# Performance work log

Measured on AMD Instinct MI355X. Metric: run time of the kernel, lower is better.

The kernel has to match this reference:

```python
import jax, jax.numpy as jnp
import numpy as np

BS, L, H, D = 4, 1024, 12, 768   # docs, seq len, attn heads, hidden
NE, M, P = 42, 96, 42 * 42        # max entities (min_height), mentions/doc, ht pairs
OFFSET = 1                        # bert/roberta [CLS] offset


def setup_inputs() -> dict:
    key = jax.random.key(0)
    k1, k2, k3, k4, k5 = jax.random.split(key, 5)
    sequence_output = jax.random.normal(k1, (BS, L, D), jnp.float32)
    attention = jax.random.uniform(k2, (BS, H, L, L), jnp.float32)
    mention_pos = jax.random.randint(k3, (BS, M), 0, L - OFFSET - 1).astype(jnp.int32)
    mention_entity = jnp.sort(jax.random.randint(k4, (BS, M), 0, NE), axis=-1).astype(jnp.int32)
    hts = jax.random.randint(k5, (BS, P, 2), 0, NE).astype(jnp.int32)
    return {"sequence_output": sequence_output, "attention": attention,
            "mention_pos": mention_pos, "mention_entity": mention_entity, "hts": hts}


def _per_doc_entities(seq, att, pos, ent):
    # seq [L,D], att [H,L,L], pos [M] mention token idx, ent [M] entity segment id
    idx = pos + OFFSET
    m_emb = seq[idx]                              # [M,D]  gathered mention embeddings
    m_att = jnp.transpose(att[:, idx], (1, 0, 2))  # [M,H,L] gathered mention attentions
    counts = jax.ops.segment_sum(jnp.ones((M,), seq.dtype), ent, num_segments=NE)
    has = counts > 0
    # mean-pool attentions per entity (zeros for empty entities, as in torch code)
    e_att = jax.ops.segment_sum(m_att, ent, num_segments=NE) / jnp.maximum(counts, 1.0)[:, None, None]
    # stable logsumexp-pool embeddings per entity
    seg_max = jax.ops.segment_max(m_emb, ent, num_segments=NE)      # -inf for empty segments
    seg_max = jnp.where(has[:, None], seg_max, 0.0)
    seg_sum = jax.ops.segment_sum(jnp.exp(m_emb - seg_max[ent]), ent, num_segments=NE)
    e_emb = jnp.where(has[:, None], jnp.log(jnp.maximum(seg_sum, 1e-30)) + seg_max, 0.0)
    return e_emb, e_att                           # [NE,D], [NE,H,L]


def _channel_map(seq, e_att):
    # all-pairs (h_att * t_att).mean(heads), normalize over tokens, contract with seq
    pair = jnp.einsum('ahl,bhl->abl', e_att, e_att) / H      # [NE,NE,L]
    pair = pair / (pair.sum(-1, keepdims=True) + 1e-5)
    return jnp.einsum('abl,ld->abd', pair, seq)              # [NE,NE,D]


def reference(sequence_output, attention, mention_pos, mention_entity, hts):
    e_emb, e_att = jax.vmap(_per_doc_entities)(sequence_output, attention,
                                               mention_pos, mention_entity)
    hss = jax.vmap(lambda emb, ht: emb[ht[:, 0]])(e_emb, hts).reshape(BS * P, D)
    tss = jax.vmap(lambda emb, ht: emb[ht[:, 1]])(e_emb, hts).reshape(BS * P, D)
    feature_map = jax.vmap(_channel_map)(sequence_output, e_att)  # [BS,NE,NE,D]
    return hss, tss, feature_map
```

## Files before the change

### kernel.cpp

```cpp
#include <hip/hip_runtime.h>
#include <hip/hip_bf16.h>

#define BSZ   4
#define LSEQ  1024
#define NH    12
#define DDIM  768
#define NEN   42
#define NM    96
#define NPAIR (NEN*NEN)
#define OFF   1

typedef short bf16x8 __attribute__((ext_vector_type(8)));
typedef float f32x4  __attribute__((ext_vector_type(4)));

__device__ __forceinline__ float bf2f(unsigned short u) {
    union { unsigned u; float f; } c; c.u = ((unsigned)u) << 16; return c.f;
}

typedef const __attribute__((address_space(1))) unsigned int glb_u32;
typedef __attribute__((address_space(3))) unsigned int lds_u32;
__device__ __forceinline__ void glds16(const void* g, void* l) {
    __builtin_amdgcn_global_load_lds((glb_u32*)g, (lds_u32*)l, 16, 0, 0);
}

#define NLC   2
#define EMB_CNT  (BSZ*NEN*DDIM)
#define PSUM_CNT (BSZ*NLC*NPAIR)
#define EATT_CNT (BSZ*NEN*NH*LSEQ)
#define PTIL_BYTES ((size_t)BSZ*NPAIR*LSEQ)

#define ATT_BLKS  (BSZ*NEN*NH)
#define T_BLKS    ((LSEQ/32)*(DDIM/32)*BSZ)
#define EMB_BLKS  (BSZ*NEN*3)
#define K1_TOTAL  (ATT_BLKS + T_BLKS + EMB_BLKS)

#define TEN   6
#define NTILE 7
#define NTRIT (NTILE*(NTILE+1)/2)
#define LCHK  512
#define PAIR_BLKS (NTRIT*NLC*BSZ)
#define GATH_BLKS (BSZ*NPAIR/4)
#define K2_TOTAL  (PAIR_BLKS + GATH_BLKS)

#define BM 128
#define BN 64
#define BK 128
#define MT 14
#define NT (DDIM/BN)
#define FMAP_BLKS (MT*NT*BSZ)

__global__ __launch_bounds__(256) void prep_kernel(
        const float* __restrict__ seq,
        const float* __restrict__ att,
        const int* __restrict__ mpos,
        const int* __restrict__ ment,
        __hip_bfloat16* __restrict__ e_att,
        unsigned char* __restrict__ seqT,
        float* __restrict__ e_emb) {
    __shared__ __align__(16) char smraw[4352];
    const int bid = blockIdx.x;
    const int t = threadIdx.x;

    if (bid < ATT_BLKS) {
        int id = bid;
        int h = id % NH;
        int e = (id / NH) % NEN;
        int b = id / (NH * NEN);
        int* sp   = (int*)smraw;
        int* se   = sp + NM;
        int* list = se + NM;
        int* pcnt = list + NM;
        if (t < NM) { sp[t] = mpos[b*NM + t] + OFF; se[t] = ment[b*NM + t]; }
        __syncthreads();
        if (t == 0) {
            int c = 0;
            for (int m = 0; m < NM; ++m) if (se[m] == e) list[c++] = sp[m];
            pcnt[0] = c;
        }
        __syncthreads();
        int cnt = pcnt[0];
        const float* ab = att + ((size_t)(b*NH + h)) * LSEQ * LSEQ;
        float4 acc = {0.f, 0.f, 0.f, 0.f};
        for (int m = 0; m < cnt; ++m) {
            float4 v = ((const float4*)(ab + (size_t)list[m]*LSEQ))[t];
            acc.x += v.x; acc.y += v.y; acc.z += v.z; acc.w += v.w;
        }
        float inv = cnt ? 1.f / (float)cnt : 0.f;
        union { ushort4 u4; __hip_bfloat16 hh[4]; } pk;
        pk.hh[0] = __float2bfloat16(acc.x * inv);
        pk.hh[1] = __float2bfloat16(acc.y * inv);
        pk.hh[2] = __float2bfloat16(acc.z * inv);
        pk.hh[3] = __float2bfloat16(acc.w * inv);
        ((ushort4*)(e_att + ((size_t)(b*NEN + e)*NH + h)*LSEQ))[t] = pk.u4;
    } else if (bid < ATT_BLKS + T_BLKS) {
        int id = bid - ATT_BLKS;
        int l0 = (id % (LSEQ/32)) * 32;
        int d0 = ((id / (LSEQ/32)) % (DDIM/32)) * 32;
        int b  = id / ((LSEQ/32) * (DDIM/32));
        float (*tile)[33] = (float(*)[33])smraw;
        int l = t >> 3, dq = (t & 7) * 4;
        float4 v = *(const float4*)(seq + ((size_t)b*LSEQ + l0 + l)*DDIM + d0 + dq);
        tile[l][dq+0] = v.x; tile[l][dq+1] = v.y;
        tile[l][dq+2] = v.z; tile[l][dq+3] = v.w;
        __syncthreads();
        int d = t >> 3, lq = (t & 7) * 4;
        int w = __builtin_amdgcn_cvt_pk_fp8_f32(tile[lq+0][d], tile[lq+1][d], 0, false);
        w     = __builtin_amdgcn_cvt_pk_fp8_f32(tile[lq+2][d], tile[lq+3][d], w, true);
        *(int*)(seqT + ((size_t)b*DDIM + d0 + d)*LSEQ + l0 + lq) = w;
    } else {
        int id = bid - ATT_BLKS - T_BLKS;
        int chunk = id % 3;
        int e = (id / 3) % NEN;
        int b = id / (3 * NEN);
        int* sp   = (int*)smraw;
        int* se   = sp + NM;
        int* list = se + NM;
        int* pcnt = list + NM;
        if (t < NM) { sp[t] = mpos[b*NM + t] + OFF; se[t] = ment[b*NM + t]; }
        __syncthreads();
        if (t == 0) {
            int c = 0;
            for (int m = 0; m < NM; ++m) if (se[m] == e) list[c++] = sp[m];
            pcnt[0] = c;
        }
        __syncthreads();
        int cnt = pcnt[0];
        int d = chunk * 256 + t;
        const float* sq = seq + (size_t)b * LSEQ * DDIM + d;
        float mx = -1e30f;
        for (int m = 0; m < cnt; ++m) mx = fmaxf(mx, sq[(size_t)list[m] * DDIM]);
        float out = 0.f;
        if (cnt) {
            float s = 0.f;
            for (int m = 0; m < cnt; ++m) s += expf(sq[(size_t)list[m] * DDIM] - mx);
            out = logf(fmaxf(s, 1e-30f)) + mx;
        }
        e_emb[((size_t)b*NEN + e)*DDIM + d] = out;
    }
}

__global__ __launch_bounds__(256) void mid_kernel(
        const __hip_bfloat16* __restrict__ e_att,
        const float* __restrict__ e_emb,
        const int* __restrict__ hts,
        unsigned char* __restrict__ ptil,
        float* __restrict__ psum,
        float* __restrict__ out_h,
        float* __restrict__ out_t) {
    __shared__ __align__(16) char smraw[640];
    const int bid = blockIdx.x;
    const int t = threadIdx.x;

    if (bid < PAIR_BLKS) {
        int tri = bid % NTRIT;
        int lc  = (bid / NTRIT) % NLC;
        int b   = bid / (NTRIT * NLC);
        int ta = 0, rem = tri;
        while (rem >= NTILE - ta) { rem -= NTILE - ta; ++ta; }
        int tb = ta + rem;
        int l = lc * LCHK + t * 2;

        const __hip_bfloat16* ebase = e_att + (size_t)b*NEN*NH*LSEQ + l;
        float sx[TEN][TEN], sy[TEN][TEN];
        #pragma unroll
        for (int i = 0; i < TEN; ++i)
            #pragma unroll
            for (int j = 0; j < TEN; ++j) { sx[i][j] = 0.f; sy[i][j] = 0.f; }

        #pragma unroll 4
        for (int h = 0; h < NH; ++h) {
            float xax[TEN], xay[TEN], xbx[TEN], xby[TEN];
            #pragma unroll
            for (int e = 0; e < TEN; ++e) {
                ushort2 u = *(const ushort2*)(ebase + ((size_t)(ta*TEN+e)*NH + h)*LSEQ);
                xax[e] = bf2f(u.x); xay[e] = bf2f(u.y);
            }
            #pragma unroll
            for (int e = 0; e < TEN; ++e) {
                ushort2 u = *(const ushort2*)(ebase + ((size_t)(tb*TEN+e)*NH + h)*LSEQ);
                xbx[e] = bf2f(u.x); xby[e] = bf2f(u.y);
            }
            #pragma unroll
            for (int i = 0; i < TEN; ++i)
                #pragma unroll
                for (int j = 0; j < TEN; ++j) {
                    sx[i][j] += xax[i] * xbx[j];
                    sy[i][j] += xay[i] * xby[j];
                }
        }

        unsigned char* pbase = ptil + (size_t)b*NPAIR*LSEQ + l;
        #pragma unroll
        for (int i = 0; i < TEN; ++i) {
            #pragma unroll
            for (int j = 0; j < TEN; ++j) {
                int w = __builtin_amdgcn_cvt_pk_fp8_f32(sx[i][j], sy[i][j], 0, false);
                unsigned short q = (unsigned short)(w & 0xFFFF);
                int pa = ta*TEN + i, pb = tb*TEN + j;
                *(unsigned short*)(pbase + (size_t)(pa*NEN + pb)*LSEQ) = q;
                if (ta != tb)
                    *(unsigned short*)(pbase + (size_t)(pb*NEN + pa)*LSEQ) = q;
            }
        }

        int lane = t & 63, w = t >> 6;
        float (*redp)[TEN*TEN] = (float(*)[TEN*TEN])smraw;
        float keep = 0.f;
        #pragma unroll
        for (int i = 0; i < TEN; ++i) {
            #pragma unroll
            for (int j = 0; j < TEN; ++j) {
                float v = sx[i][j] + sy[i][j];
                v += __shfl_xor(v,  1, 64);
                v += __shfl_xor(v,  2, 64);
                v += __shfl_xor(v,  4, 64);
                v += __shfl_xor(v,  8, 64);
                v += __shfl_xor(v, 16, 64);
                v += __shfl_xor(v, 32, 64);
                if (lane == i*TEN + j) keep = v;
            }
        }
        if (lane < TEN*TEN) redp[w][lane] = keep;
        __syncthreads();
        if (t < TEN*TEN) {
            float v = redp[0][t] + redp[1][t] + redp[2][t] + redp[3][t];
            int i = t / TEN, j = t % TEN;
            int pa = ta*TEN + i, pb = tb*TEN + j;
            float* ps = psum + ((size_t)(b*NLC + lc))*NPAIR;
            ps[pa*NEN + pb] = v;
            if (ta != tb) ps[pb*NEN + pa] = v;
        }
    } else {
        int id4  = bid - PAIR_BLKS;
        int grp  = t >> 6;
        int lane = t & 63;
        int id   = id4 * 4 + grp;
        int b    = id / NPAIR;
        int hi = hts[id*2 + 0];
        int ti = hts[id*2 + 1];
        const float4* eh = (const float4*)(e_emb + ((size_t)(b*NEN + hi))*DDIM);
        const float4* et = (const float4*)(e_emb + ((size_t)(b*NEN + ti))*DDIM);
        float4* oh = (float4*)(out_h + (size_t)id*DDIM);
        float4* ot = (float4*)(out_t + (size_t)id*DDIM);
        #pragma unroll
        for (int i = 0; i < 3; ++i) {
            oh[lane + 64*i] = eh[lane + 64*i];
            ot[lane + 64*i] = et[lane + 64*i];
        }
    }
}

__global__ __launch_bounds__(256) void gemm_kernel(
        const unsigned char* __restrict__ ptil,
        const unsigned char* __restrict__ seqT,
        const float* __restrict__ psum,
        float* __restrict__ fmap) {
    __shared__ unsigned char As[2][BM*BK];
    __shared__ unsigned char Bs[2][BN*BK];
    const int bid = blockIdx.x;
    const int t = threadIdx.x;

    int tile = (bid & 7) * (FMAP_BLKS/8) + (bid >> 3);
    const int lane = t & 63;
    const int wid  = t >> 6;
    const int wr   = wid >> 1;
    const int wc   = wid & 1;
    const int bx = tile % MT, by = (tile / MT) % NT, b = tile / (MT*NT);
    const int r0 = bx * BM, c0 = by * BN;

    const unsigned char* Ab  = ptil + (size_t)b * NPAIR * LSEQ;
    const unsigned char* Btb = seqT + (size_t)b * DDIM * LSEQ;
    unsigned char* AsB = (unsigned char*)As;
    unsigned char* BsB = (unsigned char*)Bs;

    const f32x4 zero = {0.f, 0.f, 0.f, 0.f};
    f32x4 acc[4][2];
    #pragma unroll
    for (int m = 0; m < 4; ++m)
        #pragma unroll
        for (int n = 0; n < 2; ++n) acc[m][n] = zero;

    const int fr = lane & 15, kg = lane >> 4;

#define STAGE(buf, k0)                                                        \
    {                                                                         \
        _Pragma("unroll")                                                     \
        for (int i = 0; i < 4; ++i) {                                         \
            int L = t*16 + i*4096;                                            \
            int r = L >> 7, beta = L & 127;                                   \
            glds16(Ab + (size_t)(r0 + r)*LSEQ + (k0)                          \
                      + (beta ^ ((r & 7) << 4)),                              \
                   AsB + (buf)*16384 + L);                                    \
        }                                                                     \
        _Pragma("unroll")                                                     \
        for (int i = 0; i < 2; ++i) {                                         \
            int L = t*16 + i*4096;                                            \
            int c = L >> 7, beta = L & 127;                                   \
            glds16(Btb + (size_t)(c0 + c)*LSEQ + (k0)                         \
                      + (beta ^ ((c & 7) << 4)),                              \
                   BsB + (buf)*8192 + L);                                     \
        }                                                                     \
    }

    STAGE(0, 0);
    __syncthreads();

    int cur = 0;
    for (int ki = 0; ki < LSEQ/BK; ++ki) {
        if (ki + 1 < LSEQ/BK) STAGE(cur ^ 1, (ki + 1) * BK);

        const unsigned char* Ac = AsB + cur*16384;
        const unsigned char* Bc = BsB + cur*8192;

        #pragma unroll
        for (int ks = 0; ks < 4; ++ks) {
            long af[4], bfv[2];
            #pragma unroll
            for (int m = 0; m < 4; ++m) {
                int R = wr*64 + m*16 + fr;
                int e0 = (ks*32 + kg*8) ^ ((R & 7) << 4);
                af[m] = *(const long*)(Ac + R*128 + e0);
            }
            #pragma unroll
            for (int n = 0; n < 2; ++n) {
                int C = wc*32 + n*16 + fr;
                int e0 = (ks*32 + kg*8) ^ ((C & 7) << 4);
                bfv[n] = *(const long*)(Bc + C*128 + e0);
            }
            #pragma unroll
            for (int m = 0; m < 4; ++m)
                #pragma unroll
                for (int n = 0; n < 2; ++n)
                    acc[m][n] = __builtin_amdgcn_mfma_f32_16x16x32_fp8_fp8(
                                    af[m], bfv[n], acc[m][n], 0, 0, 0);
        }
        __syncthreads();
        cur ^= 1;
    }

    const float* psb = psum + (size_t)b * NLC * NPAIR;
    #pragma unroll
    for (int m = 0; m < 4; ++m) {
        int lr0 = wr*64 + m*16 + kg*4;
        #pragma unroll
        for (int i = 0; i < 4; ++i) {
            int row = r0 + lr0 + i;
            if (row < NPAIR) {
                float S = psb[row] + psb[NPAIR + row];
                float sc = 1.f / (S + (float)NH * 1e-5f);
                #pragma unroll
                for (int n = 0; n < 2; ++n) {
                    int col = c0 + wc*32 + n*16 + fr;
                    fmap[((size_t)b*NPAIR + row)*DDIM + col] = acc[m][n][i] * sc;
                }
            }
        }
    }
#undef STAGE
}

extern "C" void kernel_launch(void* const* d_in, const int* in_sizes, int n_in,
                              void* d_out, int out_size, void* d_ws, size_t ws_size,
                              hipStream_t stream) {
    const float* seq  = (const float*)d_in[0];
    const float* att  = (const float*)d_in[1];
    const int*   mpos = (const int*)d_in[2];
    const int*   ment = (const int*)d_in[3];
    const int*   hts  = (const int*)d_in[4];

    float* ws_f  = (float*)d_ws;
    float* e_emb = ws_f;
    float* psum  = ws_f + EMB_CNT;
    __hip_bfloat16* e_att = (__hip_bfloat16*)(ws_f + EMB_CNT + PSUM_CNT);
    unsigned char* ptil = (unsigned char*)(e_att + EATT_CNT);
    unsigned char* seqT = ptil + PTIL_BYTES;

    float* out_h = (float*)d_out;
    float* out_t = out_h + (size_t)BSZ*NPAIR*DDIM;
    float* fmap  = out_t + (size_t)BSZ*NPAIR*DDIM;

    hipLaunchKernelGGL(prep_kernel, dim3(K1_TOTAL), dim3(256), 0, stream,
                       seq, att, mpos, ment, e_att, seqT, e_emb);
    hipLaunchKernelGGL(mid_kernel, dim3(K2_TOTAL), dim3(256), 0, stream,
                       e_att, e_emb, hts, ptil, psum, out_h, out_t);
    hipLaunchKernelGGL(gemm_kernel, dim3(FMAP_BLKS), dim3(256), 0, stream,
                       ptil, seqT, psum, fmap);
}
```

Baseline: 56.87 us.

## Move seq transpose into mid kernel and use partial vmcnt waits in GEMM

Result: faster. 53.51 us (-5.9%).

```diff
diff --git a/kernel.cpp b/kernel.cpp
--- a/kernel.cpp
+++ b/kernel.cpp
@@ -30,17 +30,17 @@
 #define PTIL_BYTES ((size_t)BSZ*NPAIR*LSEQ)
 
 #define ATT_BLKS  (BSZ*NEN*NH)
-#define T_BLKS    ((LSEQ/32)*(DDIM/32)*BSZ)
 #define EMB_BLKS  (BSZ*NEN*3)
-#define K1_TOTAL  (ATT_BLKS + T_BLKS + EMB_BLKS)
+#define K1_TOTAL  (ATT_BLKS + EMB_BLKS)
 
 #define TEN   6
 #define NTILE 7
 #define NTRIT (NTILE*(NTILE+1)/2)
 #define LCHK  512
 #define PAIR_BLKS (NTRIT*NLC*BSZ)
+#define T_BLKS    ((LSEQ/32)*(DDIM/32)*BSZ)
 #define GATH_BLKS (BSZ*NPAIR/4)
-#define K2_TOTAL  (PAIR_BLKS + GATH_BLKS)
+#define K2_TOTAL  (PAIR_BLKS + T_BLKS + GATH_BLKS)
 
 #define BM 128
 #define BN 64
@@ -55,21 +55,21 @@
         const int* __restrict__ mpos,
         const int* __restrict__ ment,
         __hip_bfloat16* __restrict__ e_att,
-        unsigned char* __restrict__ seqT,
         float* __restrict__ e_emb) {
-    __shared__ __align__(16) char smraw[4352];
+    __shared__ __align__(16) char smraw[1600];
     const int bid = blockIdx.x;
     const int t = threadIdx.x;
+
+    int* sp   = (int*)smraw;
+    int* se   = sp + NM;
+    int* list = se + NM;
+    int* pcnt = list + NM;
 
     if (bid < ATT_BLKS) {
         int id = bid;
         int h = id % NH;
         int e = (id / NH) % NEN;
         int b = id / (NH * NEN);
-        int* sp   = (int*)smraw;
-        int* se   = sp + NM;
-        int* list = se + NM;
-        int* pcnt = list + NM;
         if (t < NM) { sp[t] = mpos[b*NM + t] + OFF; se[t] = ment[b*NM + t]; }
         __syncthreads();
         if (t == 0) {
@@ -92,30 +92,11 @@
         pk.hh[2] = __float2bfloat16(acc.z * inv);
         pk.hh[3] = __float2bfloat16(acc.w * inv);
         ((ushort4*)(e_att + ((size_t)(b*NEN + e)*NH + h)*LSEQ))[t] = pk.u4;
-    } else if (bid < ATT_BLKS + T_BLKS) {
+    } else {
         int id = bid - ATT_BLKS;
-        int l0 = (id % (LSEQ/32)) * 32;
-        int d0 = ((id / (LSEQ/32)) % (DDIM/32)) * 32;
-        int b  = id / ((LSEQ/32) * (DDIM/32));
-        float (*tile)[33] = (float(*)[33])smraw;
-        int l = t >> 3, dq = (t & 7) * 4;
-        float4 v = *(const float4*)(seq + ((size_t)b*LSEQ + l0 + l)*DDIM + d0 + dq);
-        tile[l][dq+0] = v.x; tile[l][dq+1] = v.y;
-        tile[l][dq+2] = v.z; tile[l][dq+3] = v.w;
-        __syncthreads();
-        int d = t >> 3, lq = (t & 7) * 4;
-        int w = __builtin_amdgcn_cvt_pk_fp8_f32(tile[lq+0][d], tile[lq+1][d], 0, false);
-        w     = __builtin_amdgcn_cvt_pk_fp8_f32(tile[lq+2][d], tile[lq+3][d], w, true);
-        *(int*)(seqT + ((size_t)b*DDIM + d0 + d)*LSEQ + l0 + lq) = w;
-    } else {
-        int id = bid - ATT_BLKS - T_BLKS;
         int chunk = id % 3;
         int e = (id / 3) % NEN;
         int b = id / (3 * NEN);
-        int* sp   = (int*)smraw;
-        int* se   = sp + NM;
-        int* list = se + NM;
-        int* pcnt = list + NM;
         if (t < NM) { sp[t] = mpos[b*NM + t] + OFF; se[t] = ment[b*NM + t]; }
         __syncthreads();
         if (t == 0) {
@@ -140,14 +121,16 @@
 }
 
 __global__ __launch_bounds__(256) void mid_kernel(
+        const float* __restrict__ seq,
         const __hip_bfloat16* __restrict__ e_att,
         const float* __restrict__ e_emb,
         const int* __restrict__ hts,
         unsigned char* __restrict__ ptil,
         float* __restrict__ psum,
+        unsigned char* __restrict__ seqT,
         float* __restrict__ out_h,
         float* __restrict__ out_t) {
-    __shared__ __align__(16) char smraw[640];
+    __shared__ __align__(16) char smraw[4352];
     const int bid = blockIdx.x;
     const int t = threadIdx.x;
 
@@ -230,8 +213,23 @@
             ps[pa*NEN + pb] = v;
             if (ta != tb) ps[pb*NEN + pa] = v;
         }
+    } else if (bid < PAIR_BLKS + T_BLKS) {
+        int id = bid - PAIR_BLKS;
+        int l0 = (id % (LSEQ/32)) * 32;
+        int d0 = ((id / (LSEQ/32)) % (DDIM/32)) * 32;
+        int b  = id / ((LSEQ/32) * (DDIM/32));
+        float (*tile)[33] = (float(*)[33])smraw;
+        int l = t >> 3, dq = (t & 7) * 4;
+        float4 v = *(const float4*)(seq + ((size_t)b*LSEQ + l0 + l)*DDIM + d0 + dq);
+        tile[l][dq+0] = v.x; tile[l][dq+1] = v.y;
+        tile[l][dq+2] = v.z; tile[l][dq+3] = v.w;
+        __syncthreads();
+        int d = t >> 3, lq = (t & 7) * 4;
+        int w = __builtin_amdgcn_cvt_pk_fp8_f32(tile[lq+0][d], tile[lq+1][d], 0, false);
+        w     = __builtin_amdgcn_cvt_pk_fp8_f32(tile[lq+2][d], tile[lq+3][d], w, true);
+        *(int*)(seqT + ((size_t)b*DDIM + d0 + d)*LSEQ + l0 + lq) = w;
     } else {
-        int id4  = bid - PAIR_BLKS;
+        int id4  = bid - PAIR_BLKS - T_BLKS;
         int grp  = t >> 6;
         int lane = t & 63;
         int id   = id4 * 4 + grp;
@@ -303,11 +301,17 @@
     }
 
     STAGE(0, 0);
-    __syncthreads();
 
     int cur = 0;
     for (int ki = 0; ki < LSEQ/BK; ++ki) {
-        if (ki + 1 < LSEQ/BK) STAGE(cur ^ 1, (ki + 1) * BK);
+        if (ki + 1 < LSEQ/BK) {
+            STAGE(cur ^ 1, (ki + 1) * BK);
+            asm volatile("s_waitcnt vmcnt(6)" ::: "memory");
+        } else {
+            asm volatile("s_waitcnt vmcnt(0)" ::: "memory");
+        }
+        __builtin_amdgcn_s_barrier();
+        __builtin_amdgcn_sched_barrier(0);
 
         const unsigned char* Ac = AsB + cur*16384;
         const unsigned char* Bc = BsB + cur*8192;
@@ -334,7 +338,7 @@
                     acc[m][n] = __builtin_amdgcn_mfma_f32_16x16x32_fp8_fp8(
                                     af[m], bfv[n], acc[m][n], 0, 0, 0);
         }
-        __syncthreads();
+        __builtin_amdgcn_s_barrier();
         cur ^= 1;
     }
 
@@ -380,9 +384,9 @@
     float* fmap  = out_t + (size_t)BSZ*NPAIR*DDIM;
 
     hipLaunchKernelGGL(prep_kernel, dim3(K1_TOTAL), dim3(256), 0, stream,
-                       seq, att, mpos, ment, e_att, seqT, e_emb);
+                       seq, att, mpos, ment, e_att, e_emb);
     hipLaunchKernelGGL(mid_kernel, dim3(K2_TOTAL), dim3(256), 0, stream,
-                       e_att, e_emb, hts, ptil, psum, out_h, out_t);
+                       seq, e_att, e_emb, hts, ptil, psum, seqT, out_h, out_t);
     hipLaunchKernelGGL(gemm_kernel, dim3(FMAP_BLKS), dim3(256), 0, stream,
                        ptil, seqT, psum, fmap);
 }
```
